# Performance work log

Hardware: AMD Instinct MI355X
Metric: run time of the kernel (lower is better)

Reference implementation:

```python
import jax, jax.numpy as jnp
import numpy as np

B, S, D = 4, 2048, 2048
NH, NKV = 16, 4
HD = D // NH            # 128
DKV = NKV * HD          # 512
REP = NH // NKV         # 4
SCALE = HD ** -0.5
EPS = 1e-9


def setup_inputs() -> dict:
    key = jax.random.key(0)
    ks = jax.random.split(key, 9)
    s = 0.02
    return {
        "q": jax.random.normal(ks[0], (B, S, D), jnp.float32),
        "k": jax.random.normal(ks[1], (B, S, D), jnp.float32),
        "v": jax.random.normal(ks[2], (B, S, D), jnp.float32),
        "Wq": jax.random.normal(ks[3], (D, D), jnp.float32) * s,
        "bq": jnp.zeros((D,), jnp.float32),
        "Wk": jax.random.normal(ks[4], (D, DKV), jnp.float32) * s,
        "bk": jnp.zeros((DKV,), jnp.float32),
        "Wv": jax.random.normal(ks[5], (D, DKV), jnp.float32) * s,
        "bv": jnp.zeros((DKV,), jnp.float32),
    }


def reference(q, k, v, Wq, bq, Wk, bk, Wv, bv):
    # Dense projections (nn.Dense = x @ W + b)
    qh = q @ Wq + bq                      # (B, S, D)
    kh = k @ Wk + bk                      # (B, S, DKV)
    vh = v @ Wv + bv                      # (B, S, DKV)
    # Faithful to source: repeat along axis=-2 (the SEQUENCE axis)
    kh = jnp.repeat(kh, REP, axis=-2)     # (B, S*REP, DKV)
    vh = jnp.repeat(vh, REP, axis=-2)     # (B, S*REP, DKV)
    # flash_attention math: reshape to (B, S, NH, HD) -> (B, NH, S, HD)
    qh = qh.reshape(B, S, NH, HD).transpose(0, 2, 1, 3)
    kh = kh.reshape(B, S, NH, HD).transpose(0, 2, 1, 3)
    vh = vh.reshape(B, S, NH, HD).transpose(0, 2, 1, 3)
    attn = jnp.einsum("bhqd,bhkd->bhqk", qh, kh) * SCALE
    m = jnp.max(attn, axis=-1, keepdims=True)
    e = jnp.exp(attn - m)
    p = e / (jnp.sum(e, axis=-1, keepdims=True) + EPS)
    out = jnp.einsum("bhqk,bhkd->bhqd", p, vh)   # (B, NH, S, HD)
    return out.transpose(0, 2, 1, 3).reshape(B, S, D)
```

## Files before the change

### kernel.cpp

```cpp
#include <hip/hip_runtime.h>

#define B_    4
#define S_    2048
#define D_    2048
#define NH_   16
#define NKV_  4
#define HD_   128
#define DKV_  512
#define QSCALE_ ((float)(0.08838834764831845 * 1.4426950408889634))

typedef __attribute__((ext_vector_type(8))) short          bf16x8;
typedef __attribute__((ext_vector_type(8))) unsigned short us8;
typedef __attribute__((ext_vector_type(4))) unsigned short us4;
typedef __attribute__((ext_vector_type(4))) float          f32x4;

__device__ __forceinline__ unsigned short f2bf(float f) {
    union { float f; unsigned int u; } v; v.f = f;
    unsigned int u = v.u;
    u += 0x7fffu + ((u >> 16) & 1u);
    return (unsigned short)(u >> 16);
}

__device__ __forceinline__ unsigned int cvt_pk_bf16(float lo, float hi) {
    unsigned int r;
    asm volatile("v_cvt_pk_bf16_f32 %0, %1, %2" : "=v"(r) : "v"(lo), "v"(hi));
    return r;
}

#define GLOAD16(gp, lp) __builtin_amdgcn_global_load_lds(                      \
    (const __attribute__((address_space(1))) unsigned int*)(gp),              \
    (__attribute__((address_space(3))) unsigned int*)(lp), 16, 0, 0)

__device__ __forceinline__ void tr_body(
    const float* __restrict__ W, unsigned short* __restrict__ WT,
    int K, int N, int kb, int nb, float (*tile)[33])
{
    const int k0 = kb * 32, n0 = nb * 32;
    const int tx = threadIdx.x & 31, ty = threadIdx.x >> 5;
#pragma unroll
    for (int i = 0; i < 32; i += 8)
        tile[ty + i][tx] = W[(size_t)(k0 + ty + i) * N + n0 + tx];
    __syncthreads();
#pragma unroll
    for (int i = 0; i < 32; i += 8)
        WT[(size_t)(n0 + ty + i) * K + k0 + tx] = f2bf(tile[tx][ty + i]);
}

__global__ __launch_bounds__(256) void transpose_all(
    const float* __restrict__ Wq, const float* __restrict__ Wk,
    const float* __restrict__ Wv, unsigned short* __restrict__ WqT,
    unsigned short* __restrict__ WkT, unsigned short* __restrict__ WvT)
{
    __shared__ float tile[32][33];
    const int y = blockIdx.y;
    if (y < 64)       tr_body(Wq, WqT, D_, D_,   blockIdx.x, y,      tile);
    else if (y < 80)  tr_body(Wk, WkT, D_, DKV_, blockIdx.x, y - 64, tile);
    else              tr_body(Wv, WvT, D_, DKV_, blockIdx.x, y - 80, tile);
}

__device__ __forceinline__ void cvt_body(
    const float* __restrict__ src, unsigned short* __restrict__ dst, int n8)
{
    int i = blockIdx.x * blockDim.x + threadIdx.x;
    const int stride = gridDim.x * blockDim.x;
    const float4* p = (const float4*)src;
    us8* o8 = (us8*)dst;
    for (; i < n8; i += stride) {
        float4 a = p[2 * i], b = p[2 * i + 1];
        us8 o;
        o[0] = f2bf(a.x); o[1] = f2bf(a.y); o[2] = f2bf(a.z); o[3] = f2bf(a.w);
        o[4] = f2bf(b.x); o[5] = f2bf(b.y); o[6] = f2bf(b.z); o[7] = f2bf(b.w);
        o8[i] = o;
    }
}

__global__ __launch_bounds__(256) void cvt_bf16(
    const float* __restrict__ in, unsigned short* __restrict__ out, int n8)
{
    cvt_body(in, out, n8);
}

__global__ __launch_bounds__(256) void cvt_all(
    const float* __restrict__ q, const float* __restrict__ k,
    const float* __restrict__ v, unsigned short* __restrict__ xq,
    unsigned short* __restrict__ xk, unsigned short* __restrict__ xv)
{
    const int which = blockIdx.y;
    const float* src = which == 0 ? q : which == 1 ? k : v;
    unsigned short* dst = which == 0 ? xq : which == 1 ? xk : xv;
    cvt_body(src, dst, B_ * S_ * D_ / 8);
}

__device__ __forceinline__ void gemm_body(
    const unsigned short* __restrict__ A, const unsigned short* __restrict__ BT,
    const float* __restrict__ bias, unsigned short* __restrict__ C,
    int N, int nb, float scale, int vmode,
    unsigned short* As, unsigned short* Bs)
{
    const int K = D_;
    const int m0 = blockIdx.x * 128, n0 = nb * 128;
    const int t = threadIdx.x;
    const int w = t >> 6, l = t & 63, lr = l & 15, lg = l >> 4;
    const int wr = (w >> 1) * 64, wc = (w & 1) * 64;
    const int sr = t >> 2, sc = (t & 3) * 8;

    const unsigned short* aS = A + (size_t)(m0 + sr) * K + sc;
    const unsigned short* bS = BT + (size_t)(n0 + sr) * K + sc;

    f32x4 acc[4][4] = {};
    const int nk = K / 32;
    for (int kt = 0; kt < nk; ++kt) {
        __syncthreads();
        GLOAD16(aS + kt * 32,                    &As[t * 8]);
        GLOAD16(aS + (size_t)64 * K + kt * 32,   &As[2048 + t * 8]);
        GLOAD16(bS + kt * 32,                    &Bs[t * 8]);
        GLOAD16(bS + (size_t)64 * K + kt * 32,   &Bs[2048 + t * 8]);
        __syncthreads();

        bf16x8 af[4], bfv[4];
#pragma unroll
        for (int i = 0; i < 4; ++i)
            af[i] = *(const bf16x8*)&As[(wr + i * 16 + lr) * 32 + lg * 8];
#pragma unroll
        for (int i = 0; i < 4; ++i)
            bfv[i] = *(const bf16x8*)&Bs[(wc + i * 16 + lr) * 32 + lg * 8];
#pragma unroll
        for (int i = 0; i < 4; ++i)
#pragma unroll
            for (int j = 0; j < 4; ++j)
                acc[i][j] = __builtin_amdgcn_mfma_f32_16x16x32_bf16(
                    af[i], bfv[j], acc[i][j], 0, 0, 0);
    }

#pragma unroll
    for (int j = 0; j < 4; ++j) {
        const int col = n0 + wc + j * 16 + lr;
        const float bv = bias[col];
#pragma unroll
        for (int i = 0; i < 4; ++i) {
            const int row0 = m0 + wr + i * 16 + lg * 4;
            if (vmode == 0) {
#pragma unroll
                for (int r = 0; r < 4; ++r)
                    C[(size_t)(row0 + r) * N + col] = f2bf((acc[i][j][r] + bv) * scale);
            } else {
                const int bb = row0 >> 11, s0 = row0 & (S_ - 1);
                us4 hv;
#pragma unroll
                for (int r = 0; r < 4; ++r) hv[r] = f2bf((acc[i][j][r] + bv) * scale);
                *(us4*)&C[((size_t)bb * N + col) * S_ + s0] = hv;
            }
        }
    }
}

__global__ __launch_bounds__(256) void gemm_all(
    const unsigned short* __restrict__ xq, const unsigned short* __restrict__ xk,
    const unsigned short* __restrict__ xv,
    const unsigned short* __restrict__ WqT, const unsigned short* __restrict__ WkT,
    const unsigned short* __restrict__ WvT,
    const float* __restrict__ bq, const float* __restrict__ bk,
    const float* __restrict__ bv,
    unsigned short* __restrict__ qh, unsigned short* __restrict__ kh,
    unsigned short* __restrict__ vhT)
{
    __shared__ __align__(16) unsigned short As[128 * 32];
    __shared__ __align__(16) unsigned short Bs[128 * 32];
    const int y = blockIdx.y;
    if (y < 16)      gemm_body(xq, WqT, bq, qh,  D_,   y,      QSCALE_, 0, As, Bs);
    else if (y < 20) gemm_body(xk, WkT, bk, kh,  DKV_, y - 16, 1.0f,    0, As, Bs);
    else             gemm_body(xv, WvT, bv, vhT, DKV_, y - 20, 1.0f,    1, As, Bs);
}

__global__ __launch_bounds__(256) void gemm_lds(
    const unsigned short* __restrict__ A, const unsigned short* __restrict__ BT,
    const float* __restrict__ bias, unsigned short* __restrict__ C,
    int N, float scale, int vmode)
{
    __shared__ __align__(16) unsigned short As[128 * 32];
    __shared__ __align__(16) unsigned short Bs[128 * 32];
    gemm_body(A, BT, bias, C, N, blockIdx.y, scale, vmode, As, Bs);
}

template <int VMODE>
__global__ __launch_bounds__(256) void gemm_rs(
    const float* __restrict__ A, const unsigned short* __restrict__ BT,
    const float* __restrict__ bias, unsigned short* __restrict__ C,
    int M, int N, int K, float scale)
{
    __shared__ unsigned short As[128][40];
    __shared__ unsigned short Bs[128][40];

    const int m0 = blockIdx.x * 128, n0 = blockIdx.y * 128;
    const int t = threadIdx.x;
    const int sr = t >> 1, sc = (t & 1) * 16;
    const int w = t >> 6, l = t & 63, lr = l & 15, lg = l >> 4;
    const int wr = (w >> 1) * 64, wc = (w & 1) * 64;

    const float* aptr = A + (size_t)(m0 + sr) * K + sc;
    const unsigned short* bptr = BT + (size_t)(n0 + sr) * K + sc;

    float4 pa0, pa1, pa2, pa3;
    us8 pb0, pb1;
    auto prefetch = [&](int k0) {
        const float4* ap = (const float4*)(aptr + k0);
        pa0 = ap[0]; pa1 = ap[1]; pa2 = ap[2]; pa3 = ap[3];
        const us8* bp = (const us8*)(bptr + k0);
        pb0 = bp[0]; pb1 = bp[1];
    };

    f32x4 acc[4][4] = {};
    prefetch(0);
    const int nk = K / 32;
    for (int kt = 0; kt < nk; ++kt) {
        __syncthreads();
        us8 c0, c1;
        c0[0] = f2bf(pa0.x); c0[1] = f2bf(pa0.y); c0[2] = f2bf(pa0.z); c0[3] = f2bf(pa0.w);
        c0[4] = f2bf(pa1.x); c0[5] = f2bf(pa1.y); c0[6] = f2bf(pa1.z); c0[7] = f2bf(pa1.w);
        c1[0] = f2bf(pa2.x); c1[1] = f2bf(pa2.y); c1[2] = f2bf(pa2.z); c1[3] = f2bf(pa2.w);
        c1[4] = f2bf(pa3.x); c1[5] = f2bf(pa3.y); c1[6] = f2bf(pa3.z); c1[7] = f2bf(pa3.w);
        *(us8*)&As[sr][sc]     = c0;
        *(us8*)&As[sr][sc + 8] = c1;
        *(us8*)&Bs[sr][sc]     = pb0;
        *(us8*)&Bs[sr][sc + 8] = pb1;
        __syncthreads();
        if (kt + 1 < nk) prefetch((kt + 1) * 32);

        bf16x8 af[4], bfv[4];
#pragma unroll
        for (int i = 0; i < 4; ++i)
            af[i] = *(const bf16x8*)&As[wr + i * 16 + lr][lg * 8];
#pragma unroll
        for (int i = 0; i < 4; ++i)
            bfv[i] = *(const bf16x8*)&Bs[wc + i * 16 + lr][lg * 8];
#pragma unroll
        for (int i = 0; i < 4; ++i)
#pragma unroll
            for (int j = 0; j < 4; ++j)
                acc[i][j] = __builtin_amdgcn_mfma_f32_16x16x32_bf16(
                    af[i], bfv[j], acc[i][j], 0, 0, 0);
    }

#pragma unroll
    for (int j = 0; j < 4; ++j) {
        const int col = n0 + wc + j * 16 + lr;
        const float bv = bias[col];
#pragma unroll
        for (int i = 0; i < 4; ++i) {
            const int row0 = m0 + wr + i * 16 + lg * 4;
            if (VMODE == 0) {
#pragma unroll
                for (int r = 0; r < 4; ++r)
                    C[(size_t)(row0 + r) * N + col] = f2bf((acc[i][j][r] + bv) * scale);
            } else {
                const int bb = row0 >> 11, s0 = row0 & (S_ - 1);
                us4 hv;
#pragma unroll
                for (int r = 0; r < 4; ++r) hv[r] = f2bf((acc[i][j][r] + bv) * scale);
                *(us4*)&C[((size_t)bb * N + col) * S_ + s0] = hv;
            }
        }
    }
}

__global__ __launch_bounds__(256, 2) void attn_kernel(
    const unsigned short* __restrict__ qh, const unsigned short* __restrict__ kh,
    const unsigned short* __restrict__ vhT, float* __restrict__ out)
{
    __shared__ __align__(16) unsigned short Kd[2][64 * 128];
    __shared__ __align__(16) unsigned short Vd[2][128 * 64];
    __shared__ __align__(16) unsigned int   P2T[4][16 * 44];

    const int qb = blockIdx.x, h = blockIdx.y, b = blockIdx.z;
    const int g = h & (NKV_ - 1);
    const int t = threadIdx.x, w = t >> 6, l = t & 63, lr = l & 15, lg = l >> 4;
    const int q0 = qb * 128 + w * 32;

    bf16x8 qf[2][4];
#pragma unroll
    for (int rf = 0; rf < 2; ++rf) {
        const unsigned short* qrow =
            qh + ((size_t)(b * S_) + q0 + rf * 16 + lr) * D_ + h * HD_;
#pragma unroll
        for (int ko = 0; ko < 4; ++ko)
            qf[rf][ko] = *(const bf16x8*)(qrow + ko * 32 + lg * 8);
    }

    f32x4 o[2][8] = {};
    float mrow[2] = {-1e30f, -1e30f};
    float ls[2]   = {0.f, 0.f};

    const unsigned short* kb_ = kh + (size_t)b * S_ * DKV_ + g * HD_;
    const unsigned short* vb_ = vhT + ((size_t)b * DKV_ + g * HD_) * S_;

    const int kc = ((t & 15) * 8) ^ (((t >> 4) & 7) << 3);
    const int vc = ((t & 7) * 8) ^ (((t >> 3) & 7) << 3);

    auto stage = [&](int buf, int kt) {
        const unsigned short* ks = kb_ + (size_t)(kt * 64) * DKV_ + kc;
        const unsigned short* vs = vb_ + kt * 64 + vc;
#pragma unroll
        for (int i = 0; i < 4; ++i)
            GLOAD16(ks + (size_t)(i * 16 + (t >> 4)) * DKV_, &Kd[buf][i * 2048 + t * 8]);
#pragma unroll
        for (int i = 0; i < 4; ++i)
            GLOAD16(vs + (size_t)(i * 32 + (t >> 3)) * S_,   &Vd[buf][i * 2048 + t * 8]);
    };

    stage(0, 0);
    stage(1, 1);

    const int swz = (lr & 7) << 3;
    unsigned int* pw = &P2T[w][lr * 44];
    int cur = 0;
    const int NT = S_ / 64;
    for (int kt = 0; kt < NT; ++kt) {
        if (kt + 1 < NT) { asm volatile("s_waitcnt vmcnt(8)" ::: "memory"); }
        else             { asm volatile("s_waitcnt vmcnt(0)" ::: "memory"); }
        __builtin_amdgcn_s_barrier();
        __builtin_amdgcn_sched_barrier(0);

        f32x4 sa[2][4] = {};
        __builtin_amdgcn_s_setprio(1);
#pragma unroll
        for (int cf = 0; cf < 4; ++cf)
#pragma unroll
            for (int ko = 0; ko < 4; ++ko) {
                bf16x8 kf = *(const bf16x8*)
                    &Kd[cur][(cf * 16 + lr) * 128 + ((ko * 32 + lg * 8) ^ swz)];
                sa[0][cf] = __builtin_amdgcn_mfma_f32_16x16x32_bf16(kf, qf[0][ko], sa[0][cf], 0, 0, 0);
                sa[1][cf] = __builtin_amdgcn_mfma_f32_16x16x32_bf16(kf, qf[1][ko], sa[1][cf], 0, 0, 0);
            }
        __builtin_amdgcn_s_setprio(0);

        bf16x8 pa[2][2];
#pragma unroll
        for (int rf = 0; rf < 2; ++rf) {
            float mxl = fmaxf(fmaxf(fmaxf(sa[rf][0][0], sa[rf][0][1]),
                                    fmaxf(sa[rf][0][2], sa[rf][0][3])),
                              fmaxf(fmaxf(sa[rf][1][0], sa[rf][1][1]),
                                    fmaxf(sa[rf][1][2], sa[rf][1][3])));
            mxl = fmaxf(mxl, fmaxf(fmaxf(fmaxf(sa[rf][2][0], sa[rf][2][1]),
                                         fmaxf(sa[rf][2][2], sa[rf][2][3])),
                                   fmaxf(fmaxf(sa[rf][3][0], sa[rf][3][1]),
                                         fmaxf(sa[rf][3][2], sa[rf][3][3]))));
            float m = mrow[rf];
            if (!__all(mxl <= m + 8.f)) {
                float mx = fmaxf(mxl, m);
                mx = fmaxf(mx, __shfl_xor(mx, 16));
                mx = fmaxf(mx, __shfl_xor(mx, 32));
                const float al = exp2f(m - mx);
                mrow[rf] = m = mx;
                ls[rf] *= al;
#pragma unroll
                for (int r = 0; r < 4; ++r) {
                    const float a = __shfl(al, lg * 4 + r);
#pragma unroll
                    for (int df = 0; df < 8; ++df) o[rf][df][r] *= a;
                }
            }
            float p[4][4];
#pragma unroll
            for (int cf = 0; cf < 4; ++cf)
#pragma unroll
                for (int r = 0; r < 4; ++r)
                    p[cf][r] = exp2f(sa[rf][cf][r] - m);
            ls[rf] += ((p[0][0] + p[0][1]) + (p[0][2] + p[0][3]))
                    + ((p[1][0] + p[1][1]) + (p[1][2] + p[1][3]))
                    + ((p[2][0] + p[2][1]) + (p[2][2] + p[2][3]))
                    + ((p[3][0] + p[3][1]) + (p[3][2] + p[3][3]));
#pragma unroll
            for (int cf = 0; cf < 4; ++cf) {
                uint2 pk;
                pk.x = cvt_pk_bf16(p[cf][0], p[cf][1]);
                pk.y = cvt_pk_bf16(p[cf][2], p[cf][3]);
                *(uint2*)&pw[cf * 8 + lg * 2] = pk;
            }
            pa[rf][0] = *(const bf16x8*)&pw[lg * 4];
            pa[rf][1] = *(const bf16x8*)&pw[16 + lg * 4];
        }

        __builtin_amdgcn_s_setprio(1);
#pragma unroll
        for (int ks = 0; ks < 2; ++ks)
#pragma unroll
            for (int df = 0; df < 8; ++df) {
                bf16x8 vf = *(const bf16x8*)
                    &Vd[cur][(df * 16 + lr) * 64 + ((ks * 32 + lg * 8) ^ swz)];
                o[0][df] = __builtin_amdgcn_mfma_f32_16x16x32_bf16(pa[0][ks], vf, o[0][df], 0, 0, 0);
                o[1][df] = __builtin_amdgcn_mfma_f32_16x16x32_bf16(pa[1][ks], vf, o[1][df], 0, 0, 0);
            }
        __builtin_amdgcn_s_setprio(0);

        __builtin_amdgcn_sched_barrier(0);
        __builtin_amdgcn_s_barrier();
        __builtin_amdgcn_sched_barrier(0);
        if (kt + 2 < NT) stage(cur, kt + 2);
        cur ^= 1;
    }

#pragma unroll
    for (int rf = 0; rf < 2; ++rf) {
        float lst = ls[rf];
        lst += __shfl_xor(lst, 16);
        lst += __shfl_xor(lst, 32);
        const float inv = 1.f / (lst + 1e-9f);
        float* ob = out + ((size_t)(b * S_) + q0 + rf * 16 + lg * 4) * D_ + h * HD_;
#pragma unroll
        for (int r = 0; r < 4; ++r) {
            const float ivr = __shfl(inv, lg * 4 + r);
#pragma unroll
            for (int df = 0; df < 8; ++df)
                ob[(size_t)r * D_ + df * 16 + lr] = o[rf][df][r] * ivr;
        }
    }
}

extern "C" void kernel_launch(void* const* d_in, const int* in_sizes, int n_in,
                              void* d_out, int out_size, void* d_ws, size_t ws_size,
                              hipStream_t stream)
{
    const float* q  = (const float*)d_in[0];
    const float* k  = (const float*)d_in[1];
    const float* v  = (const float*)d_in[2];
    const float* Wq = (const float*)d_in[3];
    const float* bq = (const float*)d_in[4];
    const float* Wk = (const float*)d_in[5];
    const float* bk = (const float*)d_in[6];
    const float* Wv = (const float*)d_in[7];
    const float* bv = (const float*)d_in[8];
    float* out = (float*)d_out;

    char* ws = (char*)d_ws;
    unsigned short* qh  = (unsigned short*)ws; ws += (size_t)B_ * S_ * D_ * 2;
    unsigned short* kh  = (unsigned short*)ws; ws += (size_t)B_ * S_ * DKV_ * 2;
    unsigned short* vhT = (unsigned short*)ws; ws += (size_t)B_ * DKV_ * S_ * 2;
    unsigned short* WqT = (unsigned short*)ws; ws += (size_t)D_ * D_ * 2;
    unsigned short* WkT = (unsigned short*)ws; ws += (size_t)DKV_ * D_ * 2;
    unsigned short* WvT = (unsigned short*)ws; ws += (size_t)DKV_ * D_ * 2;
    unsigned short* xq  = (unsigned short*)ws; ws += (size_t)B_ * S_ * D_ * 2;
    unsigned short* xk  = (unsigned short*)ws; ws += (size_t)B_ * S_ * D_ * 2;
    unsigned short* xv  = (unsigned short*)ws; ws += (size_t)B_ * S_ * D_ * 2;

    const size_t need3 = (size_t)163577856;
    const size_t need1 = (size_t)96468992;

    transpose_all<<<dim3(64, 96), 256, 0, stream>>>(Wq, Wk, Wv, WqT, WkT, WvT);

    const int M = B_ * S_;
    const int n8 = M * D_ / 8;

    if (ws_size >= need3) {
        cvt_all<<<dim3(1024, 3), 256, 0, stream>>>(q, k, v, xq, xk, xv);
        gemm_all<<<dim3(M / 128, 24), 256, 0, stream>>>(
            xq, xk, xv, WqT, WkT, WvT, bq, bk, bv, qh, kh, vhT);
    } else if (ws_size >= need1) {
        cvt_bf16<<<2048, 256, 0, stream>>>(q, xq, n8);
        gemm_lds<<<dim3(M / 128, D_ / 128), 256, 0, stream>>>(xq, WqT, bq, qh, D_, QSCALE_, 0);
        cvt_bf16<<<2048, 256, 0, stream>>>(k, xq, n8);
        gemm_lds<<<dim3(M / 128, DKV_ / 128), 256, 0, stream>>>(xq, WkT, bk, kh, DKV_, 1.0f, 0);
        cvt_bf16<<<2048, 256, 0, stream>>>(v, xq, n8);
        gemm_lds<<<dim3(M / 128, DKV_ / 128), 256, 0, stream>>>(xq, WvT, bv, vhT, DKV_, 1.0f, 1);
    } else {
        gemm_rs<0><<<dim3(M / 128, D_ / 128), 256, 0, stream>>>(q, WqT, bq, qh, M, D_, D_, QSCALE_);
        gemm_rs<0><<<dim3(M / 128, DKV_ / 128), 256, 0, stream>>>(k, WkT, bk, kh, M, DKV_, D_, 1.0f);
        gemm_rs<1><<<dim3(M / 128, DKV_ / 128), 256, 0, stream>>>(v, WvT, bv, vhT, M, DKV_, D_, 1.0f);
    }

    attn_kernel<<<dim3(S_ / 128, NH_, B_), 256, 0, stream>>>(qh, kh, vhT, out);
}
```

Baseline: 414.5 us.

## Fuse fp32-to-bf16 input conversion into projection GEMM and use MFMA row sums

The projection GEMM now reads fp32 activations directly, converts them to bf16 in registers with packed conversion, and writes them to padded LDS, replacing the separate conversion kernel and its bf16 staging buffers. The attention kernel computes the softmax row sums with an extra MFMA against a ones vector instead of scalar adds and cross-lane shuffles, and uses v_max3 for the row max. This removes a full extra read and write pass over the inputs and some VALU work. In exchange the GEMM's A operand is loaded through registers rather than asynchronous direct-to-LDS loads, and the attention kernel issues extra MFMAs.

```diff
diff --git a/kernel.cpp b/kernel.cpp
--- a/kernel.cpp
+++ b/kernel.cpp
@@ -27,6 +27,12 @@
     return r;
 }
 
+__device__ __forceinline__ float vmax3(float a, float b, float c) {
+    float r;
+    asm("v_max3_f32 %0, %1, %2, %3" : "=v"(r) : "v"(a), "v"(b), "v"(c));
+    return r;
+}
+
 #define GLOAD16(gp, lp) __builtin_amdgcn_global_load_lds(                      \
     (const __attribute__((address_space(1))) unsigned int*)(gp),              \
     (__attribute__((address_space(3))) unsigned int*)(lp), 16, 0, 0)
@@ -58,69 +64,52 @@
     else              tr_body(Wv, WvT, D_, DKV_, blockIdx.x, y - 80, tile);
 }
 
-__device__ __forceinline__ void cvt_body(
-    const float* __restrict__ src, unsigned short* __restrict__ dst, int n8)
-{
-    int i = blockIdx.x * blockDim.x + threadIdx.x;
-    const int stride = gridDim.x * blockDim.x;
-    const float4* p = (const float4*)src;
-    us8* o8 = (us8*)dst;
-    for (; i < n8; i += stride) {
-        float4 a = p[2 * i], b = p[2 * i + 1];
-        us8 o;
-        o[0] = f2bf(a.x); o[1] = f2bf(a.y); o[2] = f2bf(a.z); o[3] = f2bf(a.w);
-        o[4] = f2bf(b.x); o[5] = f2bf(b.y); o[6] = f2bf(b.z); o[7] = f2bf(b.w);
-        o8[i] = o;
-    }
-}
-
-__global__ __launch_bounds__(256) void cvt_bf16(
-    const float* __restrict__ in, unsigned short* __restrict__ out, int n8)
-{
-    cvt_body(in, out, n8);
-}
-
-__global__ __launch_bounds__(256) void cvt_all(
-    const float* __restrict__ q, const float* __restrict__ k,
-    const float* __restrict__ v, unsigned short* __restrict__ xq,
-    unsigned short* __restrict__ xk, unsigned short* __restrict__ xv)
-{
-    const int which = blockIdx.y;
-    const float* src = which == 0 ? q : which == 1 ? k : v;
-    unsigned short* dst = which == 0 ? xq : which == 1 ? xk : xv;
-    cvt_body(src, dst, B_ * S_ * D_ / 8);
-}
-
 __device__ __forceinline__ void gemm_body(
-    const unsigned short* __restrict__ A, const unsigned short* __restrict__ BT,
+    const float* __restrict__ A, const unsigned short* __restrict__ BT,
     const float* __restrict__ bias, unsigned short* __restrict__ C,
     int N, int nb, float scale, int vmode,
-    unsigned short* As, unsigned short* Bs)
+    unsigned short* As , unsigned short* Bs )
 {
     const int K = D_;
     const int m0 = blockIdx.x * 128, n0 = nb * 128;
     const int t = threadIdx.x;
     const int w = t >> 6, l = t & 63, lr = l & 15, lg = l >> 4;
     const int wr = (w >> 1) * 64, wc = (w & 1) * 64;
-    const int sr = t >> 2, sc = (t & 3) * 8;
-
-    const unsigned short* aS = A + (size_t)(m0 + sr) * K + sc;
-    const unsigned short* bS = BT + (size_t)(n0 + sr) * K + sc;
+    const int srA = t >> 1, scA = (t & 1) * 16;
+    const int srB = t >> 2, scB = (t & 3) * 8;
+
+    const float* aptr = A + (size_t)(m0 + srA) * K + scA;
+    const unsigned short* bS = BT + (size_t)(n0 + srB) * K + scB;
+
+    float4 pa0, pa1, pa2, pa3;
+    auto prefA = [&](int k0) {
+        const float4* ap = (const float4*)(aptr + k0);
+        pa0 = ap[0]; pa1 = ap[1]; pa2 = ap[2]; pa3 = ap[3];
+    };
 
     f32x4 acc[4][4] = {};
+    prefA(0);
     const int nk = K / 32;
     for (int kt = 0; kt < nk; ++kt) {
         __syncthreads();
-        GLOAD16(aS + kt * 32,                    &As[t * 8]);
-        GLOAD16(aS + (size_t)64 * K + kt * 32,   &As[2048 + t * 8]);
-        GLOAD16(bS + kt * 32,                    &Bs[t * 8]);
-        GLOAD16(bS + (size_t)64 * K + kt * 32,   &Bs[2048 + t * 8]);
+        GLOAD16(bS + kt * 32,                  &Bs[t * 8]);
+        GLOAD16(bS + (size_t)64 * K + kt * 32, &Bs[2048 + t * 8]);
+        uint2 c0, c1;
+        c0.x = cvt_pk_bf16(pa0.x, pa0.y); c0.y = cvt_pk_bf16(pa0.z, pa0.w);
+        c1.x = cvt_pk_bf16(pa1.x, pa1.y); c1.y = cvt_pk_bf16(pa1.z, pa1.w);
+        *(uint2*)&As[srA * 40 + scA]     = c0;
+        *(uint2*)&As[srA * 40 + scA + 4] = c1;
+        c0.x = cvt_pk_bf16(pa2.x, pa2.y); c0.y = cvt_pk_bf16(pa2.z, pa2.w);
+        c1.x = cvt_pk_bf16(pa3.x, pa3.y); c1.y = cvt_pk_bf16(pa3.z, pa3.w);
+        *(uint2*)&As[srA * 40 + scA + 8]  = c0;
+        *(uint2*)&As[srA * 40 + scA + 12] = c1;
         __syncthreads();
+        if (kt + 1 < nk) prefA((kt + 1) * 32);
 
         bf16x8 af[4], bfv[4];
 #pragma unroll
         for (int i = 0; i < 4; ++i)
-            af[i] = *(const bf16x8*)&As[(wr + i * 16 + lr) * 32 + lg * 8];
+            af[i] = *(const bf16x8*)&As[(wr + i * 16 + lr) * 40 + lg * 8];
 #pragma unroll
         for (int i = 0; i < 4; ++i)
             bfv[i] = *(const bf16x8*)&Bs[(wc + i * 16 + lr) * 32 + lg * 8];
@@ -155,8 +144,8 @@
 }
 
 __global__ __launch_bounds__(256) void gemm_all(
-    const unsigned short* __restrict__ xq, const unsigned short* __restrict__ xk,
-    const unsigned short* __restrict__ xv,
+    const float* __restrict__ q, const float* __restrict__ k,
+    const float* __restrict__ v,
     const unsigned short* __restrict__ WqT, const unsigned short* __restrict__ WkT,
     const unsigned short* __restrict__ WvT,
     const float* __restrict__ bq, const float* __restrict__ bk,
@@ -164,103 +153,12 @@
     unsigned short* __restrict__ qh, unsigned short* __restrict__ kh,
     unsigned short* __restrict__ vhT)
 {
-    __shared__ __align__(16) unsigned short As[128 * 32];
+    __shared__ __align__(16) unsigned short As[128 * 40];
     __shared__ __align__(16) unsigned short Bs[128 * 32];
     const int y = blockIdx.y;
-    if (y < 16)      gemm_body(xq, WqT, bq, qh,  D_,   y,      QSCALE_, 0, As, Bs);
-    else if (y < 20) gemm_body(xk, WkT, bk, kh,  DKV_, y - 16, 1.0f,    0, As, Bs);
-    else             gemm_body(xv, WvT, bv, vhT, DKV_, y - 20, 1.0f,    1, As, Bs);
-}
-
-__global__ __launch_bounds__(256) void gemm_lds(
-    const unsigned short* __restrict__ A, const unsigned short* __restrict__ BT,
-    const float* __restrict__ bias, unsigned short* __restrict__ C,
-    int N, float scale, int vmode)
-{
-    __shared__ __align__(16) unsigned short As[128 * 32];
-    __shared__ __align__(16) unsigned short Bs[128 * 32];
-    gemm_body(A, BT, bias, C, N, blockIdx.y, scale, vmode, As, Bs);
-}
-
-template <int VMODE>
-__global__ __launch_bounds__(256) void gemm_rs(
-    const float* __restrict__ A, const unsigned short* __restrict__ BT,
-    const float* __restrict__ bias, unsigned short* __restrict__ C,
-    int M, int N, int K, float scale)
-{
-    __shared__ unsigned short As[128][40];
-    __shared__ unsigned short Bs[128][40];
-
-    const int m0 = blockIdx.x * 128, n0 = blockIdx.y * 128;
-    const int t = threadIdx.x;
-    const int sr = t >> 1, sc = (t & 1) * 16;
-    const int w = t >> 6, l = t & 63, lr = l & 15, lg = l >> 4;
-    const int wr = (w >> 1) * 64, wc = (w & 1) * 64;
-
-    const float* aptr = A + (size_t)(m0 + sr) * K + sc;
-    const unsigned short* bptr = BT + (size_t)(n0 + sr) * K + sc;
-
-    float4 pa0, pa1, pa2, pa3;
-    us8 pb0, pb1;
-    auto prefetch = [&](int k0) {
-        const float4* ap = (const float4*)(aptr + k0);
-        pa0 = ap[0]; pa1 = ap[1]; pa2 = ap[2]; pa3 = ap[3];
-        const us8* bp = (const us8*)(bptr + k0);
-        pb0 = bp[0]; pb1 = bp[1];
-    };
-
-    f32x4 acc[4][4] = {};
-    prefetch(0);
-    const int nk = K / 32;
-    for (int kt = 0; kt < nk; ++kt) {
-        __syncthreads();
-        us8 c0, c1;
-        c0[0] = f2bf(pa0.x); c0[1] = f2bf(pa0.y); c0[2] = f2bf(pa0.z); c0[3] = f2bf(pa0.w);
-        c0[4] = f2bf(pa1.x); c0[5] = f2bf(pa1.y); c0[6] = f2bf(pa1.z); c0[7] = f2bf(pa1.w);
-        c1[0] = f2bf(pa2.x); c1[1] = f2bf(pa2.y); c1[2] = f2bf(pa2.z); c1[3] = f2bf(pa2.w);
-        c1[4] = f2bf(pa3.x); c1[5] = f2bf(pa3.y); c1[6] = f2bf(pa3.z); c1[7] = f2bf(pa3.w);
-        *(us8*)&As[sr][sc]     = c0;
-        *(us8*)&As[sr][sc + 8] = c1;
-        *(us8*)&Bs[sr][sc]     = pb0;
-        *(us8*)&Bs[sr][sc + 8] = pb1;
-        __syncthreads();
-        if (kt + 1 < nk) prefetch((kt + 1) * 32);
-
-        bf16x8 af[4], bfv[4];
-#pragma unroll
-        for (int i = 0; i < 4; ++i)
-            af[i] = *(const bf16x8*)&As[wr + i * 16 + lr][lg * 8];
-#pragma unroll
-        for (int i = 0; i < 4; ++i)
-            bfv[i] = *(const bf16x8*)&Bs[wc + i * 16 + lr][lg * 8];
-#pragma unroll
-        for (int i = 0; i < 4; ++i)
-#pragma unroll
-            for (int j = 0; j < 4; ++j)
-                acc[i][j] = __builtin_amdgcn_mfma_f32_16x16x32_bf16(
-                    af[i], bfv[j], acc[i][j], 0, 0, 0);
-    }
-
-#pragma unroll
-    for (int j = 0; j < 4; ++j) {
-        const int col = n0 + wc + j * 16 + lr;
-        const float bv = bias[col];
-#pragma unroll
-        for (int i = 0; i < 4; ++i) {
-            const int row0 = m0 + wr + i * 16 + lg * 4;
-            if (VMODE == 0) {
-#pragma unroll
-                for (int r = 0; r < 4; ++r)
-                    C[(size_t)(row0 + r) * N + col] = f2bf((acc[i][j][r] + bv) * scale);
-            } else {
-                const int bb = row0 >> 11, s0 = row0 & (S_ - 1);
-                us4 hv;
-#pragma unroll
-                for (int r = 0; r < 4; ++r) hv[r] = f2bf((acc[i][j][r] + bv) * scale);
-                *(us4*)&C[((size_t)bb * N + col) * S_ + s0] = hv;
-            }
-        }
-    }
+    if (y < 16)      gemm_body(q, WqT, bq, qh,  D_,   y,      QSCALE_, 0, As, Bs);
+    else if (y < 20) gemm_body(k, WkT, bk, kh,  DKV_, y - 16, 1.0f,    0, As, Bs);
+    else             gemm_body(v, WvT, bv, vhT, DKV_, y - 20, 1.0f,    1, As, Bs);
 }
 
 __global__ __launch_bounds__(256, 2) void attn_kernel(
@@ -286,9 +184,13 @@
             qf[rf][ko] = *(const bf16x8*)(qrow + ko * 32 + lg * 8);
     }
 
+    bf16x8 onesf;
+#pragma unroll
+    for (int j = 0; j < 8; ++j) onesf[j] = (short)0x3F80;
+
     f32x4 o[2][8] = {};
+    f32x4 oe[2] = {};
     float mrow[2] = {-1e30f, -1e30f};
-    float ls[2]   = {0.f, 0.f};
 
     const unsigned short* kb_ = kh + (size_t)b * S_ * DKV_ + g * HD_;
     const unsigned short* vb_ = vhT + ((size_t)b * DKV_ + g * HD_) * S_;
@@ -336,14 +238,13 @@
         bf16x8 pa[2][2];
 #pragma unroll
         for (int rf = 0; rf < 2; ++rf) {
-            float mxl = fmaxf(fmaxf(fmaxf(sa[rf][0][0], sa[rf][0][1]),
-                                    fmaxf(sa[rf][0][2], sa[rf][0][3])),
-                              fmaxf(fmaxf(sa[rf][1][0], sa[rf][1][1]),
-                                    fmaxf(sa[rf][1][2], sa[rf][1][3])));
-            mxl = fmaxf(mxl, fmaxf(fmaxf(fmaxf(sa[rf][2][0], sa[rf][2][1]),
-                                         fmaxf(sa[rf][2][2], sa[rf][2][3])),
-                                   fmaxf(fmaxf(sa[rf][3][0], sa[rf][3][1]),
-                                         fmaxf(sa[rf][3][2], sa[rf][3][3]))));
+            const float m0v = vmax3(sa[rf][0][0], sa[rf][0][1], sa[rf][0][2]);
+            const float m1v = vmax3(sa[rf][0][3], sa[rf][1][0], sa[rf][1][1]);
+            const float m2v = vmax3(sa[rf][1][2], sa[rf][1][3], sa[rf][2][0]);
+            const float m3v = vmax3(sa[rf][2][1], sa[rf][2][2], sa[rf][2][3]);
+            const float m4v = vmax3(sa[rf][3][0], sa[rf][3][1], sa[rf][3][2]);
+            const float mxl = fmaxf(vmax3(m0v, m1v, m2v),
+                                    vmax3(m3v, m4v, sa[rf][3][3]));
             float m = mrow[rf];
             if (!__all(mxl <= m + 8.f)) {
                 float mx = fmaxf(mxl, m);
@@ -351,10 +252,10 @@
                 mx = fmaxf(mx, __shfl_xor(mx, 32));
                 const float al = exp2f(m - mx);
                 mrow[rf] = m = mx;
-                ls[rf] *= al;
 #pragma unroll
                 for (int r = 0; r < 4; ++r) {
                     const float a = __shfl(al, lg * 4 + r);
+                    oe[rf][r] *= a;
 #pragma unroll
                     for (int df = 0; df < 8; ++df) o[rf][df][r] *= a;
                 }
@@ -365,10 +266,6 @@
 #pragma unroll
                 for (int r = 0; r < 4; ++r)
                     p[cf][r] = exp2f(sa[rf][cf][r] - m);
-            ls[rf] += ((p[0][0] + p[0][1]) + (p[0][2] + p[0][3]))
-                    + ((p[1][0] + p[1][1]) + (p[1][2] + p[1][3]))
-                    + ((p[2][0] + p[2][1]) + (p[2][2] + p[2][3]))
-                    + ((p[3][0] + p[3][1]) + (p[3][2] + p[3][3]));
 #pragma unroll
             for (int cf = 0; cf < 4; ++cf) {
                 uint2 pk;
@@ -390,6 +287,10 @@
                 o[0][df] = __builtin_amdgcn_mfma_f32_16x16x32_bf16(pa[0][ks], vf, o[0][df], 0, 0, 0);
                 o[1][df] = __builtin_amdgcn_mfma_f32_16x16x32_bf16(pa[1][ks], vf, o[1][df], 0, 0, 0);
             }
+        oe[0] = __builtin_amdgcn_mfma_f32_16x16x32_bf16(pa[0][0], onesf, oe[0], 0, 0, 0);
+        oe[0] = __builtin_amdgcn_mfma_f32_16x16x32_bf16(pa[0][1], onesf, oe[0], 0, 0, 0);
+        oe[1] = __builtin_amdgcn_mfma_f32_16x16x32_bf16(pa[1][0], onesf, oe[1], 0, 0, 0);
+        oe[1] = __builtin_amdgcn_mfma_f32_16x16x32_bf16(pa[1][1], onesf, oe[1], 0, 0, 0);
         __builtin_amdgcn_s_setprio(0);
 
         __builtin_amdgcn_sched_barrier(0);
@@ -401,17 +302,13 @@
 
 #pragma unroll
     for (int rf = 0; rf < 2; ++rf) {
-        float lst = ls[rf];
-        lst += __shfl_xor(lst, 16);
-        lst += __shfl_xor(lst, 32);
-        const float inv = 1.f / (lst + 1e-9f);
         float* ob = out + ((size_t)(b * S_) + q0 + rf * 16 + lg * 4) * D_ + h * HD_;
 #pragma unroll
         for (int r = 0; r < 4; ++r) {
-            const float ivr = __shfl(inv, lg * 4 + r);
+            const float inv = 1.f / (oe[rf][r] + 1e-9f);
 #pragma unroll
             for (int df = 0; df < 8; ++df)
-                ob[(size_t)r * D_ + df * 16 + lr] = o[rf][df][r] * ivr;
+                ob[(size_t)r * D_ + df * 16 + lr] = o[rf][df][r] * inv;
         }
     }
 }
@@ -438,34 +335,12 @@
     unsigned short* WqT = (unsigned short*)ws; ws += (size_t)D_ * D_ * 2;
     unsigned short* WkT = (unsigned short*)ws; ws += (size_t)DKV_ * D_ * 2;
     unsigned short* WvT = (unsigned short*)ws; ws += (size_t)DKV_ * D_ * 2;
-    unsigned short* xq  = (unsigned short*)ws; ws += (size_t)B_ * S_ * D_ * 2;
-    unsigned short* xk  = (unsigned short*)ws; ws += (size_t)B_ * S_ * D_ * 2;
-    unsigned short* xv  = (unsigned short*)ws; ws += (size_t)B_ * S_ * D_ * 2;
-
-    const size_t need3 = (size_t)163577856;
-    const size_t need1 = (size_t)96468992;
 
     transpose_all<<<dim3(64, 96), 256, 0, stream>>>(Wq, Wk, Wv, WqT, WkT, WvT);
 
     const int M = B_ * S_;
-    const int n8 = M * D_ / 8;
-
-    if (ws_size >= need3) {
-        cvt_all<<<dim3(1024, 3), 256, 0, stream>>>(q, k, v, xq, xk, xv);
-        gemm_all<<<dim3(M / 128, 24), 256, 0, stream>>>(
-            xq, xk, xv, WqT, WkT, WvT, bq, bk, bv, qh, kh, vhT);
-    } else if (ws_size >= need1) {
-        cvt_bf16<<<2048, 256, 0, stream>>>(q, xq, n8);
-        gemm_lds<<<dim3(M / 128, D_ / 128), 256, 0, stream>>>(xq, WqT, bq, qh, D_, QSCALE_, 0);
-        cvt_bf16<<<2048, 256, 0, stream>>>(k, xq, n8);
-        gemm_lds<<<dim3(M / 128, DKV_ / 128), 256, 0, stream>>>(xq, WkT, bk, kh, DKV_, 1.0f, 0);
-        cvt_bf16<<<2048, 256, 0, stream>>>(v, xq, n8);
-        gemm_lds<<<dim3(M / 128, DKV_ / 128), 256, 0, stream>>>(xq, WvT, bv, vhT, DKV_, 1.0f, 1);
-    } else {
-        gemm_rs<0><<<dim3(M / 128, D_ / 128), 256, 0, stream>>>(q, WqT, bq, qh, M, D_, D_, QSCALE_);
-        gemm_rs<0><<<dim3(M / 128, DKV_ / 128), 256, 0, stream>>>(k, WkT, bk, kh, M, DKV_, D_, 1.0f);
-        gemm_rs<1><<<dim3(M / 128, DKV_ / 128), 256, 0, stream>>>(v, WvT, bv, vhT, M, DKV_, D_, 1.0f);
-    }
+    gemm_all<<<dim3(M / 128, 24), 256, 0, stream>>>(
+        q, k, v, WqT, WkT, WvT, bq, bk, bv, qh, kh, vhT);
 
     attn_kernel<<<dim3(S_ / 128, NH_, B_), 256, 0, stream>>>(qh, kh, vhT, out);
 }
```

New measurement: 395.0 us. 4.7% less time.
